# Kernel optimization log

Measured on AMD Instinct MI355X. Metric: run time of the kernel, lower is better.

## Reference

```python
import jax, jax.numpy as jnp
import numpy as np

L, B, C, H = 1024, 8, 1024, 16
D = C // H  # 64


def setup_inputs() -> dict:
    key = jax.random.key(0)
    ks = jax.random.split(key, 8)
    hidden_states = jax.random.normal(ks[0], (L, B, C), dtype=jnp.float32)
    rotary_pos_emb = jax.random.uniform(ks[1], (L, D // 2), dtype=jnp.float32) * 10.0
    attention_mask = jax.random.randint(ks[2], (B, L, L), 0, 2) > 0
    s = 1.0 / np.sqrt(C)
    Wqkv = jax.random.uniform(ks[3], (3 * C, C), dtype=jnp.float32, minval=-s, maxval=s)
    bqkv = jax.random.uniform(ks[4], (3 * C,), dtype=jnp.float32, minval=-s, maxval=s)
    Wo = jax.random.uniform(ks[5], (C, C), dtype=jnp.float32, minval=-s, maxval=s)
    bo = jax.random.uniform(ks[6], (C,), dtype=jnp.float32, minval=-s, maxval=s)
    return {"hidden_states": hidden_states, "rotary_pos_emb": rotary_pos_emb,
            "attention_mask": attention_mask, "Wqkv": Wqkv, "bqkv": bqkv, "Wo": Wo, "bo": bo}


def _rotate_half(x):
    # interleaved pairs: [-x1, x0, -x3, x2, ...]
    x2 = x.reshape(*x.shape[:-1], -1, 2)
    return jnp.stack((-x2[..., 1], x2[..., 0]), axis=-1).reshape(x.shape)


def reference(hidden_states, rotary_pos_emb, attention_mask, Wqkv, bqkv, Wo, bo):
    Lx, Bx, Cx = hidden_states.shape
    # QKV projection: (L,B,3C) -> (3,B,L,H,D)
    qkv = hidden_states @ Wqkv.T + bqkv
    qkv = qkv.reshape(Lx, Bx, 3, H, D).transpose(2, 1, 0, 3, 4)
    q, k, v = qkv[0], qkv[1], qkv[2]  # (B, L, H, D)
    # RoPE: freqs (L, D/2) -> cos/sin (1, L, 1, D) via duplication
    rpe = rotary_pos_emb[None] if rotary_pos_emb.ndim == 2 else rotary_pos_emb
    cos = jnp.concatenate([jnp.cos(rpe), jnp.cos(rpe)], axis=-1)[:, :, None, :]
    sin = jnp.concatenate([jnp.sin(rpe), jnp.sin(rpe)], axis=-1)[:, :, None, :]
    q = q * cos + _rotate_half(q) * sin
    k = k * cos + _rotate_half(k) * sin
    # (B, H, L, D)
    q = q.transpose(0, 2, 1, 3)
    k = k.transpose(0, 2, 1, 3)
    v = v.transpose(0, 2, 1, 3)
    scale = 1.0 / jnp.sqrt(jnp.asarray(D, dtype=q.dtype))
    scores = jnp.einsum('bhqd,bhkd->bhqk', q, k) * scale
    # torch SDPA bool mask: True = attend, False = masked
    scores = jnp.where(attention_mask[:, None, :, :], scores, jnp.finfo(scores.dtype).min)
    attn = jax.nn.softmax(scores, axis=-1)
    out = jnp.einsum('bhqk,bhkd->bhqd', attn, v)  # (B, H, L, D)
    out = out.transpose(2, 0, 1, 3).reshape(Lx, Bx, Cx)  # (L, B, C)
    return out @ Wo.T + bo
```

## Files before the change

### kernel.cpp

```cpp
#include <hip/hip_runtime.h>
#include <hip/hip_bf16.h>

typedef short bf16x8 __attribute__((ext_vector_type(8)));
typedef short bf16x4 __attribute__((ext_vector_type(4)));
typedef float f32x4 __attribute__((ext_vector_type(4)));
typedef unsigned int u32;
typedef unsigned long long u64;

#define GLD_LDS16(gp, lp) \
  __builtin_amdgcn_global_load_lds((const __attribute__((address_space(1))) u32*)(gp), \
                                   (__attribute__((address_space(3))) u32*)(lp), 16, 0, 0)

__device__ __forceinline__ short f2bf(float f) {
  u32 u = __builtin_bit_cast(u32, f);
  u = (u + 0x7fffu + ((u >> 16) & 1u)) >> 16;
  return (short)u;
}

__device__ __forceinline__ u32 pack2_bf16(float a, float b) {
#if __has_builtin(__builtin_amdgcn_cvt_pk_bf16_f32)
  typedef __bf16 bf16v2 __attribute__((ext_vector_type(2)));
  bf16v2 r = __builtin_amdgcn_cvt_pk_bf16_f32(a, b);
  return __builtin_bit_cast(u32, r);
#else
  u32 r;
  asm("v_cvt_pk_bf16_f32 %0, %1, %2" : "=v"(r) : "v"(a), "v"(b));
  return r;
#endif
}

__device__ __forceinline__ float exp2_fast(float x) {
#if __has_builtin(__builtin_amdgcn_exp2f)
  return __builtin_amdgcn_exp2f(x);
#else
  return exp2f(x);
#endif
}

__global__ __launch_bounds__(256) void prep_all(
    const int* __restrict__ m, u64* __restrict__ maskb,
    const float* __restrict__ hs, const float* __restrict__ wqkv,
    const float* __restrict__ wo, short* __restrict__ xb,
    short* __restrict__ wqkvb, short* __restrict__ wob,
    const float* __restrict__ rpe, float* __restrict__ cosT,
    float* __restrict__ sinT) {
  int b = blockIdx.x;
  if (b < 32768) {
    int i = b * 256 + threadIdx.x;
    u64 bm = __ballot(m[i] != 0);
    if ((threadIdx.x & 63) == 0) maskb[i >> 6] = bm;
    return;
  }
  b -= 32768;
  if (b < 12288) {
    const float* in;
    short* out;
    int base;
    if (b < 8192) {
      in = hs; out = xb; base = b * 1024;
    } else if (b < 8192 + 3072) {
      in = wqkv; out = wqkvb; base = (b - 8192) * 1024;
    } else {
      in = wo; out = wob; base = (b - 11264) * 1024;
    }
    int i = base + threadIdx.x * 4;
    float4 v = *(const float4*)(in + i);
    short4 o;
    o.x = f2bf(v.x); o.y = f2bf(v.y); o.z = f2bf(v.z); o.w = f2bf(v.w);
    *(short4*)(out + i) = o;
    return;
  }
  b -= 12288;
  int i = b * 256 + threadIdx.x;
  float v = rpe[i];
  cosT[i] = cosf(v);
  sinT[i] = sinf(v);
}

__global__ __launch_bounds__(512, 2) void gemm_qkv(
    const short* __restrict__ Xb, const short* __restrict__ Wb,
    const float* __restrict__ bqkv, const float* __restrict__ cosT,
    const float* __restrict__ sinT, short* __restrict__ qb,
    short* __restrict__ kbuf, short* __restrict__ vbuf) {
  __shared__ short lds[3][24576];
  const int tid = threadIdx.x;
  const int wid = tid >> 6, lane = tid & 63;
  const int g = lane >> 4, c = lane & 15;
  const int wm = wid >> 2, wn = wid & 3;
  const int bid = blockIdx.y * 12 + blockIdx.x;
  const int swz = (bid & 7) * 96 + (bid >> 3);
  const int m0 = (swz / 12) * 128, n0 = (swz % 12) * 256;

  f32x4 acc[4][4];
#pragma unroll
  for (int i = 0; i < 4; i++)
#pragma unroll
    for (int j = 0; j < 4; j++) acc[i][j] = (f32x4){0.f, 0.f, 0.f, 0.f};

  const int trow = tid >> 3;
  const int gch = ((tid & 7) ^ (trow & 7)) * 8;
  const short* Ag = Xb + (long)(m0 + trow) * 1024 + gch;
  const short* Bg = Wb + (long)(n0 + trow) * 1024 + gch;
  const int lo = tid * 8;

  const int fA = (wm * 64 + c) * 64;
  const int fB = 8192 + (wn * 64 + c) * 64;
  const int ck0 = (g ^ (c & 7)) * 8;

#define QKV_STG(bs, ko) do { \
    GLD_LDS16(Ag + (ko),              &lds[bs][lo]); \
    GLD_LDS16(Ag + (ko) + 64 * 1024,  &lds[bs][4096 + lo]); \
    GLD_LDS16(Bg + (ko),              &lds[bs][8192 + lo]); \
    GLD_LDS16(Bg + (ko) + 64 * 1024,  &lds[bs][12288 + lo]); \
    GLD_LDS16(Bg + (ko) + 128 * 1024, &lds[bs][16384 + lo]); \
    GLD_LDS16(Bg + (ko) + 192 * 1024, &lds[bs][20480 + lo]); \
  } while (0)

  QKV_STG(0, 0);
  QKV_STG(1, 64);
  asm volatile("s_waitcnt vmcnt(6)" ::: "memory");
  __builtin_amdgcn_s_barrier();

  bf16x8 fa[2][4], fb[2][4];
#pragma unroll
  for (int mf = 0; mf < 4; mf++) fa[0][mf] = *(const bf16x8*)&lds[0][fA + mf * 1024 + ck0];
#pragma unroll
  for (int nf = 0; nf < 4; nf++) fb[0][nf] = *(const bf16x8*)&lds[0][fB + nf * 1024 + ck0];

#pragma unroll
  for (int kt = 0; kt < 16; ++kt) {
    const short* Bf = &lds[kt % 3][0];
#pragma unroll
    for (int mf = 0; mf < 4; mf++) fa[1][mf] = *(const bf16x8*)&Bf[fA + mf * 1024 + (ck0 ^ 32)];
#pragma unroll
    for (int nf = 0; nf < 4; nf++) fb[1][nf] = *(const bf16x8*)&Bf[fB + nf * 1024 + (ck0 ^ 32)];
    __builtin_amdgcn_sched_barrier(0);
    __builtin_amdgcn_s_setprio(1);
#pragma unroll
    for (int mf = 0; mf < 4; mf++)
#pragma unroll
      for (int nf = 0; nf < 4; nf++)
        acc[mf][nf] = __builtin_amdgcn_mfma_f32_16x16x32_bf16(fb[0][nf], fa[0][mf], acc[mf][nf], 0, 0, 0);
    __builtin_amdgcn_s_setprio(0);
    __builtin_amdgcn_sched_barrier(0);
    if (kt < 15) {
      asm volatile("s_waitcnt vmcnt(0)" ::: "memory");
      __builtin_amdgcn_s_barrier();
      if (kt < 14) QKV_STG((kt + 2) % 3, (kt + 2) * 64);
      const short* Bn = &lds[(kt + 1) % 3][0];
#pragma unroll
      for (int mf = 0; mf < 4; mf++) fa[0][mf] = *(const bf16x8*)&Bn[fA + mf * 1024 + ck0];
#pragma unroll
      for (int nf = 0; nf < 4; nf++) fb[0][nf] = *(const bf16x8*)&Bn[fB + nf * 1024 + ck0];
      __builtin_amdgcn_sched_barrier(0);
    }
    __builtin_amdgcn_s_setprio(1);
#pragma unroll
    for (int mf = 0; mf < 4; mf++)
#pragma unroll
      for (int nf = 0; nf < 4; nf++)
        acc[mf][nf] = __builtin_amdgcn_mfma_f32_16x16x32_bf16(fb[1][nf], fa[1][mf], acc[mf][nf], 0, 0, 0);
    __builtin_amdgcn_s_setprio(0);
  }
#undef QKV_STG

  for (int jt = 0; jt < 4; jt++) {
    const int chan = n0 + wn * 64 + jt * 16 + g * 4;
    const int three = chan >> 10;
    const int hh = (chan >> 6) & 15;
    const int d = chan & 63;
    const float4 bq = *(const float4*)&bqkv[chan];
    for (int i = 0; i < 4; i++) {
      const int r = m0 + wm * 64 + i * 16 + c;
      const int l = r >> 3, b = r & 7;
      float v0 = acc[i][jt][0] + bq.x;
      float v1 = acc[i][jt][1] + bq.y;
      float v2 = acc[i][jt][2] + bq.z;
      float v3 = acc[i][jt][3] + bq.w;
      const long doff = ((long)(b * 16 + hh) * 1024 + l) * 64 + d;
      if (three == 2) {
        uint2 o = {pack2_bf16(v0, v1), pack2_bf16(v2, v3)};
        *(uint2*)&vbuf[doff] = o;
      } else {
        const float4 cs = *(const float4*)&cosT[l * 32 + (d & 31)];
        const float4 sn = *(const float4*)&sinT[l * 32 + (d & 31)];
        float e0 = v0 * cs.x - v1 * sn.x;
        float o0 = v1 * cs.y + v0 * sn.y;
        float e1 = v2 * cs.z - v3 * sn.z;
        float o1 = v3 * cs.w + v2 * sn.w;
        short* dst;
        if (three == 0) {
          const float S = 0.18033688011f;
          e0 *= S; o0 *= S; e1 *= S; o1 *= S;
          dst = qb;
        } else {
          dst = kbuf;
        }
        uint2 o = {pack2_bf16(e0, o0), pack2_bf16(e1, o1)};
        *(uint2*)&dst[doff] = o;
      }
    }
  }
}

__global__ __launch_bounds__(256) void transpose_v(const short* __restrict__ vbuf,
                                                   short* __restrict__ vTb) {
  __shared__ short T[64 * 72];
  const int bh = blockIdx.y;
  const int l0 = blockIdx.x * 64;
  const int t = threadIdx.x;
  const int row = t >> 3;
  const int cc = (t & 7) * 8;
  const short* src = vbuf + ((long)bh * 1024 + l0) * 64;
  for (int p = 0; p < 2; p++) {
    int lr = row + p * 32;
    *(bf16x8*)&T[lr * 72 + cc] = *(const bf16x8*)&src[(long)lr * 64 + cc];
  }
  __syncthreads();
  short* dst = vTb + (long)bh * 64 * 1024 + l0;
  for (int p = 0; p < 2; p++) {
    int d = row + p * 32;
    bf16x8 v;
    for (int j = 0; j < 8; j++) v[j] = T[(cc + j) * 72 + d];
    *(bf16x8*)&dst[(long)d * 1024 + cc] = v;
  }
}

__global__ __launch_bounds__(256, 5) void flash_attn(
    const short* __restrict__ qb, const short* __restrict__ kbuf,
    const short* __restrict__ vTb, const u64* __restrict__ maskb,
    short* __restrict__ attno) {
  __shared__ short K0[64 * 64], K1[64 * 64];
  __shared__ short V0[64 * 64], V1[64 * 64];
  const int t = threadIdx.x;
  const int wid = t >> 6, lane = t & 63;
  const int g = lane >> 4, c = lane & 15;
  const int bid = blockIdx.y * 16 + blockIdx.x;
  const int swz = (bid & 7) * 256 + (bid >> 3);
  const int q0 = (swz & 15) * 64;
  const int bh = swz >> 4;
  const int b = bh >> 4;
  const int h = bh & 15;
  const long qoff = (long)bh * 1024 * 64;
  const int qrow = q0 + wid * 16 + c;

  bf16x8 aq0, aq1;
  {
    const short* qp = qb + qoff + (long)qrow * 64;
    aq0 = *(const bf16x8*)(qp + g * 8);
    aq1 = *(const bf16x8*)(qp + 32 + g * 8);
  }

  f32x4 Od[4];
  for (int i = 0; i < 4; i++) Od[i] = (f32x4){0.f, 0.f, 0.f, 0.f};
  f32x4 Ld = (f32x4){0.f, 0.f, 0.f, 0.f};
  float m_run = -1e30f;

  bf16x8 avOnes8;
  {
    union { bf16x8 v; u32 u[4]; } av;
    u32 o1 = (c == 0) ? 0x3F803F80u : 0u;
    av.u[0] = av.u[1] = av.u[2] = av.u[3] = o1;
    avOnes8 = av.v;
  }

  const u64* mrow = maskb + ((long)b * 1024 + qrow) * 16;
  const short* Kg = kbuf + qoff;
  const short* Vg = vTb + qoff;

  const int l8 = lane >> 3, l7 = lane & 7;
  const int sr = wid * 16 + l8;
  const int sch = ((l7 ^ l8) & 7) * 8;
  const int r1 = wid * 16 + l8;
  const int r2 = r1 + 8;
  const int kp1 = (r1 & 32) | (((r1 & 15) >> 2) << 3) | (((r1 >> 4) & 1) << 2) | (r1 & 3);
  const int kp2 = (r2 & 32) | (((r2 & 15) >> 2) << 3) | (((r2 >> 4) & 1) << 2) | (r2 & 3);

  const int ck0 = g ^ (c & 7);
  const int kOff0 = c * 64 + ck0 * 8;
  const int kOff1 = c * 64 + (ck0 ^ 4) * 8;
  int vOff32[2];
  for (int kg = 0; kg < 2; kg++)
    vOff32[kg] = c * 64 + (((kg * 4 + g) ^ (c & 7)) * 8);

#define STAGE(KD, VD, ktn) do { \
    GLD_LDS16(Kg + (long)((ktn) + kp1) * 64 + sch,      &KD[(wid * 16) * 64]); \
    GLD_LDS16(Kg + (long)((ktn) + kp2) * 64 + sch,      &KD[(wid * 16 + 8) * 64]); \
    GLD_LDS16(Vg + (long)sr * 1024 + (ktn) + sch,       &VD[(wid * 16) * 64]); \
    GLD_LDS16(Vg + (long)(sr + 8) * 1024 + (ktn) + sch, &VD[(wid * 16 + 8) * 64]); \
  } while (0)

#define TILE(KB, VB, KP, VP, ki) do { \
    u64 mw = mrow[ki]; \
    __syncthreads(); \
    STAGE(KP, VP, (((ki) + 1) & 15) * 64); \
    f32x4 z[4]; \
    for (int nt = 0; nt < 4; nt++) { \
      bf16x8 bk0 = *(const bf16x8*)&KB[kOff0 + nt * 1024]; \
      bf16x8 bk1 = *(const bf16x8*)&KB[kOff1 + nt * 1024]; \
      f32x4 zz = (f32x4){0.f, 0.f, 0.f, 0.f}; \
      zz = __builtin_amdgcn_mfma_f32_16x16x32_bf16(bk0, aq0, zz, 0, 0, 0); \
      zz = __builtin_amdgcn_mfma_f32_16x16x32_bf16(bk1, aq1, zz, 0, 0, 0); \
      z[nt] = zz; \
    } \
    float mx = fmaxf(fmaxf(fmaxf(z[0][0], z[0][1]), fmaxf(z[0][2], z[0][3])), \
                     fmaxf(fmaxf(z[1][0], z[1][1]), fmaxf(z[1][2], z[1][3]))); \
    mx = fmaxf(mx, fmaxf(fmaxf(fmaxf(z[2][0], z[2][1]), fmaxf(z[2][2], z[2][3])), \
                         fmaxf(fmaxf(z[3][0], z[3][1]), fmaxf(z[3][2], z[3][3])))); \
    if (__ballot(mx > m_run + 8.f)) { \
      mx = fmaxf(mx, __shfl_xor(mx, 16, 64)); \
      mx = fmaxf(mx, __shfl_xor(mx, 32, 64)); \
      float mnew = fmaxf(m_run, mx); \
      float al = exp2_fast(m_run - mnew); \
      for (int dt = 0; dt < 4; dt++) { \
        Od[dt][0] *= al; Od[dt][1] *= al; Od[dt][2] *= al; Od[dt][3] *= al; \
      } \
      Ld[0] *= al; \
      m_run = mnew; \
    } \
    for (int kg = 0; kg < 2; kg++) { \
      union { bf16x8 v; u32 u[4]; } pu; \
      for (int ntp = 0; ntp < 2; ntp++) { \
        const int nt = kg * 2 + ntp; \
        u32 m4 = (u32)(mw >> (kg * 32 + g * 8 + ntp * 4)) & 0xFu; \
        u32 mlo = ((m4 & 1u) ? 0xFFFFu : 0u) | ((m4 & 2u) ? 0xFFFF0000u : 0u); \
        u32 mhi = ((m4 & 4u) ? 0xFFFFu : 0u) | ((m4 & 8u) ? 0xFFFF0000u : 0u); \
        float p0 = exp2_fast(z[nt][0] - m_run); \
        float p1 = exp2_fast(z[nt][1] - m_run); \
        float p2 = exp2_fast(z[nt][2] - m_run); \
        float p3 = exp2_fast(z[nt][3] - m_run); \
        pu.u[ntp * 2 + 0] = pack2_bf16(p0, p1) & mlo; \
        pu.u[ntp * 2 + 1] = pack2_bf16(p2, p3) & mhi; \
      } \
      Ld = __builtin_amdgcn_mfma_f32_16x16x32_bf16(avOnes8, pu.v, Ld, 0, 0, 0); \
      for (int dt = 0; dt < 4; dt++) { \
        bf16x8 av = *(const bf16x8*)&VB[vOff32[kg] + dt * 1024]; \
        Od[dt] = __builtin_amdgcn_mfma_f32_16x16x32_bf16(av, pu.v, Od[dt], 0, 0, 0); \
      } \
    } \
  } while (0)

  STAGE(K0, V0, 0);
  for (int ki = 0; ki < 16; ki += 2) {
    TILE(K0, V0, K1, V1, ki);
    TILE(K1, V1, K0, V0, ki + 1);
  }
#undef TILE
#undef STAGE

  float lsum = __shfl(Ld[0], c, 64);
  float inv = 1.f / lsum;
  long rbase = ((long)qrow * 8 + b) * 1024 + h * 64 + g * 4;
  for (int dt = 0; dt < 4; dt++) {
    union { bf16x4 v; u32 u[2]; } o;
    o.u[0] = pack2_bf16(Od[dt][0] * inv, Od[dt][1] * inv);
    o.u[1] = pack2_bf16(Od[dt][2] * inv, Od[dt][3] * inv);
    *(bf16x4*)&attno[rbase + dt * 16] = o.v;
  }
}

__global__ __launch_bounds__(256, 3) void gemm_out(
    const short* __restrict__ Ab, const short* __restrict__ Wob,
    const float* __restrict__ bo, float* __restrict__ out) {
  __shared__ short Ash[3][4096];
  __shared__ short Bsh[3][4096];
  const int tid = threadIdx.x;
  const int wid = tid >> 6, lane = tid & 63;
  const int g = lane >> 4, c = lane & 15;
  const int wm = wid >> 1, wn = wid & 1;
  const int bid = blockIdx.y * 8 + blockIdx.x;
  const int swz = (bid & 7) * 64 + (bid >> 3);
  const int m0 = (swz >> 3) * 128, n0 = (swz & 7) * 128;

  f32x4 acc[4][4];
#pragma unroll
  for (int i = 0; i < 4; i++)
#pragma unroll
    for (int j = 0; j < 4; j++) acc[i][j] = (f32x4){0.f, 0.f, 0.f, 0.f};

  const int srow = lane >> 2;
  const int scol = ((lane & 3) ^ ((lane >> 3) & 3)) * 8;
  const short* AgL = Ab + (long)(m0 + wid * 32 + srow) * 1024 + scol;
  const short* BgL = Wob + (long)(n0 + wid * 32 + srow) * 1024 + scol;
  const int dst0 = (wid * 32) * 32;
  const int dst1 = (wid * 32 + 16) * 32;
  const int ck = g ^ ((c >> 1) & 3);

#define OUT_STG(bs, ko) do { \
    GLD_LDS16(AgL + (ko), &Ash[bs][dst0]); \
    GLD_LDS16(AgL + (ko) + 16 * 1024, &Ash[bs][dst1]); \
    GLD_LDS16(BgL + (ko), &Bsh[bs][dst0]); \
    GLD_LDS16(BgL + (ko) + 16 * 1024, &Bsh[bs][dst1]); \
  } while (0)

  OUT_STG(0, 0);
  OUT_STG(1, 32);
  asm volatile("s_waitcnt vmcnt(4)" ::: "memory");
  __builtin_amdgcn_s_barrier();

  bf16x8 af[2][4], bfr[2][4];
#pragma unroll
  for (int i = 0; i < 4; i++)
    af[0][i] = *(const bf16x8*)&Ash[0][(wm * 64 + i * 16 + c) * 32 + ck * 8];
#pragma unroll
  for (int j = 0; j < 4; j++)
    bfr[0][j] = *(const bf16x8*)&Bsh[0][(wn * 64 + j * 16 + c) * 32 + ck * 8];

#pragma unroll
  for (int kt = 0; kt < 32; ++kt) {
    const int cur = kt & 1, nxt = cur ^ 1;
    __builtin_amdgcn_s_setprio(1);
#pragma unroll
    for (int i = 0; i < 2; i++)
#pragma unroll
      for (int j = 0; j < 4; j++)
        acc[i][j] = __builtin_amdgcn_mfma_f32_16x16x32_bf16(af[cur][i], bfr[cur][j], acc[i][j], 0, 0, 0);
    __builtin_amdgcn_s_setprio(0);
    __builtin_amdgcn_sched_barrier(0);
    if (kt < 31) {
      asm volatile("s_waitcnt vmcnt(0)" ::: "memory");
      __builtin_amdgcn_s_barrier();
      if (kt < 30) OUT_STG((kt + 2) % 3, (kt + 2) * 32);
      const int bn = (kt + 1) % 3;
#pragma unroll
      for (int i = 0; i < 4; i++)
        af[nxt][i] = *(const bf16x8*)&Ash[bn][(wm * 64 + i * 16 + c) * 32 + ck * 8];
#pragma unroll
      for (int j = 0; j < 4; j++)
        bfr[nxt][j] = *(const bf16x8*)&Bsh[bn][(wn * 64 + j * 16 + c) * 32 + ck * 8];
      __builtin_amdgcn_sched_barrier(0);
    }
    __builtin_amdgcn_s_setprio(1);
#pragma unroll
    for (int i = 2; i < 4; i++)
#pragma unroll
      for (int j = 0; j < 4; j++)
        acc[i][j] = __builtin_amdgcn_mfma_f32_16x16x32_bf16(af[cur][i], bfr[cur][j], acc[i][j], 0, 0, 0);
    __builtin_amdgcn_s_setprio(0);
  }
#undef OUT_STG

  for (int jt = 0; jt < 4; jt++) {
    const int j = n0 + wn * 64 + jt * 16 + c;
    const float bias = bo[j];
    for (int i = 0; i < 4; i++) {
      const int rbase = m0 + wm * 64 + i * 16 + g * 4;
      for (int reg = 0; reg < 4; reg++)
        out[(long)(rbase + reg) * 1024 + j] = acc[i][jt][reg] + bias;
    }
  }
}

extern "C" void kernel_launch(void* const* d_in, const int* in_sizes, int n_in,
                              void* d_out, int out_size, void* d_ws, size_t ws_size,
                              hipStream_t stream) {
  const float* hs = (const float*)d_in[0];
  const float* rpe = (const float*)d_in[1];
  const int* amask = (const int*)d_in[2];
  const float* Wqkv = (const float*)d_in[3];
  const float* bqkv = (const float*)d_in[4];
  const float* Wo = (const float*)d_in[5];
  const float* bo = (const float*)d_in[6];
  float* out = (float*)d_out;

  char* ws = (char*)d_ws;
  auto alloc = [&](size_t bytes) {
    char* p = ws;
    ws += (bytes + 255) & ~(size_t)255;
    return p;
  };
  short* Xb = (short*)alloc(8192LL * 1024 * 2);
  short* Wqkvb = (short*)alloc(3072LL * 1024 * 2);
  short* Wob = (short*)alloc(1024LL * 1024 * 2);
  float* cosT = (float*)alloc(1024 * 32 * 4);
  float* sinT = (float*)alloc(1024 * 32 * 4);
  u64* maskb = (u64*)alloc(8LL * 1024 * 16 * 8);
  short* qb = (short*)alloc(128LL * 1024 * 64 * 2);
  short* kbuf = (short*)alloc(128LL * 1024 * 64 * 2);
  short* vbuf = (short*)alloc(128LL * 1024 * 64 * 2);
  short* vTb = (short*)alloc(128LL * 1024 * 64 * 2);
  short* attno = (short*)alloc(8192LL * 1024 * 2);

  prep_all<<<45184, 256, 0, stream>>>(amask, maskb, hs, Wqkv, Wo, Xb, Wqkvb, Wob,
                                      rpe, cosT, sinT);
  gemm_qkv<<<dim3(12, 64), 512, 0, stream>>>(Xb, Wqkvb, bqkv, cosT, sinT, qb, kbuf, vbuf);
  transpose_v<<<dim3(16, 128), 256, 0, stream>>>(vbuf, vTb);
  flash_attn<<<dim3(16, 128), 256, 0, stream>>>(qb, kbuf, vTb, maskb, attno);
  gemm_out<<<dim3(8, 64), 256, 0, stream>>>(attno, Wob, bo, out);
}
```

Baseline: 304.3 us.

## Store attention mask as bytes and expand with v_perm in flash attention

The prep kernel now converts the int mask to one byte per element using vectorized int4 loads, replacing the ballot-packed bitmask. Flash attention reads 8 mask bytes per row segment and expands them into bf16 lane masks with v_perm_b32, instead of the shift/select bit logic. It also adds s_setprio around the MFMA sections and reorders P computation into two full groups. The trade-off is that the mask buffer grows 8x (8 MB versus 1 MB), which adds global reads inside the attention loop in exchange for cheaper ALU work and fewer prep blocks.

```diff
diff --git a/kernel.cpp b/kernel.cpp
--- a/kernel.cpp
+++ b/kernel.cpp
@@ -37,21 +37,32 @@
 #endif
 }
 
+__device__ __forceinline__ u32 bytemask2(u32 src, u32 sel) {
+  u32 r;
+  asm("v_perm_b32 %0, %1, %1, %2" : "=v"(r) : "v"(src), "v"(sel));
+  return r;
+}
+
 __global__ __launch_bounds__(256) void prep_all(
-    const int* __restrict__ m, u64* __restrict__ maskb,
+    const int* __restrict__ m, unsigned char* __restrict__ maskt,
     const float* __restrict__ hs, const float* __restrict__ wqkv,
     const float* __restrict__ wo, short* __restrict__ xb,
     short* __restrict__ wqkvb, short* __restrict__ wob,
     const float* __restrict__ rpe, float* __restrict__ cosT,
     float* __restrict__ sinT) {
   int b = blockIdx.x;
-  if (b < 32768) {
-    int i = b * 256 + threadIdx.x;
-    u64 bm = __ballot(m[i] != 0);
-    if ((threadIdx.x & 63) == 0) maskb[i >> 6] = bm;
+  if (b < 8192) {
+    int i = b * 1024 + threadIdx.x * 4;
+    int4 v = *(const int4*)(m + i);
+    uchar4 o;
+    o.x = v.x ? 0xFFu : 0u;
+    o.y = v.y ? 0xFFu : 0u;
+    o.z = v.z ? 0xFFu : 0u;
+    o.w = v.w ? 0xFFu : 0u;
+    *(uchar4*)(maskt + i) = o;
     return;
   }
-  b -= 32768;
+  b -= 8192;
   if (b < 12288) {
     const float* in;
     short* out;
@@ -228,7 +239,7 @@
 
 __global__ __launch_bounds__(256, 5) void flash_attn(
     const short* __restrict__ qb, const short* __restrict__ kbuf,
-    const short* __restrict__ vTb, const u64* __restrict__ maskb,
+    const short* __restrict__ vTb, const unsigned char* __restrict__ maskt,
     short* __restrict__ attno) {
   __shared__ short K0[64 * 64], K1[64 * 64];
   __shared__ short V0[64 * 64], V1[64 * 64];
@@ -244,6 +255,9 @@
   const long qoff = (long)bh * 1024 * 64;
   const int qrow = q0 + wid * 16 + c;
 
+  const u32 SEL01 = 0x01010000u;
+  const u32 SEL23 = 0x03030202u;
+
   bf16x8 aq0, aq1;
   {
     const short* qp = qb + qoff + (long)qrow * 64;
@@ -264,7 +278,7 @@
     avOnes8 = av.v;
   }
 
-  const u64* mrow = maskb + ((long)b * 1024 + qrow) * 16;
+  const unsigned char* mrow8 = maskt + ((long)b * 1024 + qrow) * 1024 + g * 8;
   const short* Kg = kbuf + qoff;
   const short* Vg = vTb + qoff;
 
@@ -291,10 +305,13 @@
   } while (0)
 
 #define TILE(KB, VB, KP, VP, ki) do { \
-    u64 mw = mrow[ki]; \
-    __syncthreads(); \
+    __syncthreads();  \
     STAGE(KP, VP, (((ki) + 1) & 15) * 64); \
+     \
+    const uint2 w0 = *(const uint2*)&mrow8[(ki) * 64]; \
+    const uint2 w1 = *(const uint2*)&mrow8[(ki) * 64 + 32]; \
     f32x4 z[4]; \
+    __builtin_amdgcn_s_setprio(1); \
     for (int nt = 0; nt < 4; nt++) { \
       bf16x8 bk0 = *(const bf16x8*)&KB[kOff0 + nt * 1024]; \
       bf16x8 bk1 = *(const bf16x8*)&KB[kOff1 + nt * 1024]; \
@@ -303,11 +320,12 @@
       zz = __builtin_amdgcn_mfma_f32_16x16x32_bf16(bk1, aq1, zz, 0, 0, 0); \
       z[nt] = zz; \
     } \
+    __builtin_amdgcn_s_setprio(0); \
     float mx = fmaxf(fmaxf(fmaxf(z[0][0], z[0][1]), fmaxf(z[0][2], z[0][3])), \
                      fmaxf(fmaxf(z[1][0], z[1][1]), fmaxf(z[1][2], z[1][3]))); \
     mx = fmaxf(mx, fmaxf(fmaxf(fmaxf(z[2][0], z[2][1]), fmaxf(z[2][2], z[2][3])), \
                          fmaxf(fmaxf(z[3][0], z[3][1]), fmaxf(z[3][2], z[3][3])))); \
-    if (__ballot(mx > m_run + 8.f)) { \
+    if (__ballot(mx > m_run + 8.f)) {  \
       mx = fmaxf(mx, __shfl_xor(mx, 16, 64)); \
       mx = fmaxf(mx, __shfl_xor(mx, 32, 64)); \
       float mnew = fmaxf(m_run, mx); \
@@ -318,26 +336,39 @@
       Ld[0] *= al; \
       m_run = mnew; \
     } \
-    for (int kg = 0; kg < 2; kg++) { \
-      union { bf16x8 v; u32 u[4]; } pu; \
-      for (int ntp = 0; ntp < 2; ntp++) { \
-        const int nt = kg * 2 + ntp; \
-        u32 m4 = (u32)(mw >> (kg * 32 + g * 8 + ntp * 4)) & 0xFu; \
-        u32 mlo = ((m4 & 1u) ? 0xFFFFu : 0u) | ((m4 & 2u) ? 0xFFFF0000u : 0u); \
-        u32 mhi = ((m4 & 4u) ? 0xFFFFu : 0u) | ((m4 & 8u) ? 0xFFFF0000u : 0u); \
-        float p0 = exp2_fast(z[nt][0] - m_run); \
-        float p1 = exp2_fast(z[nt][1] - m_run); \
-        float p2 = exp2_fast(z[nt][2] - m_run); \
-        float p3 = exp2_fast(z[nt][3] - m_run); \
-        pu.u[ntp * 2 + 0] = pack2_bf16(p0, p1) & mlo; \
-        pu.u[ntp * 2 + 1] = pack2_bf16(p2, p3) & mhi; \
-      } \
-      Ld = __builtin_amdgcn_mfma_f32_16x16x32_bf16(avOnes8, pu.v, Ld, 0, 0, 0); \
-      for (int dt = 0; dt < 4; dt++) { \
-        bf16x8 av = *(const bf16x8*)&VB[vOff32[kg] + dt * 1024]; \
-        Od[dt] = __builtin_amdgcn_mfma_f32_16x16x32_bf16(av, pu.v, Od[dt], 0, 0, 0); \
-      } \
+    union { bf16x8 v; u32 u[4]; } puA, puB; \
+    { \
+      float p0 = exp2_fast(z[0][0] - m_run), p1 = exp2_fast(z[0][1] - m_run); \
+      float p2 = exp2_fast(z[0][2] - m_run), p3 = exp2_fast(z[0][3] - m_run); \
+      float p4 = exp2_fast(z[1][0] - m_run), p5 = exp2_fast(z[1][1] - m_run); \
+      float p6 = exp2_fast(z[1][2] - m_run), p7 = exp2_fast(z[1][3] - m_run); \
+      puA.u[0] = pack2_bf16(p0, p1) & bytemask2(w0.x, SEL01); \
+      puA.u[1] = pack2_bf16(p2, p3) & bytemask2(w0.x, SEL23); \
+      puA.u[2] = pack2_bf16(p4, p5) & bytemask2(w0.y, SEL01); \
+      puA.u[3] = pack2_bf16(p6, p7) & bytemask2(w0.y, SEL23); \
     } \
+    { \
+      float p0 = exp2_fast(z[2][0] - m_run), p1 = exp2_fast(z[2][1] - m_run); \
+      float p2 = exp2_fast(z[2][2] - m_run), p3 = exp2_fast(z[2][3] - m_run); \
+      float p4 = exp2_fast(z[3][0] - m_run), p5 = exp2_fast(z[3][1] - m_run); \
+      float p6 = exp2_fast(z[3][2] - m_run), p7 = exp2_fast(z[3][3] - m_run); \
+      puB.u[0] = pack2_bf16(p0, p1) & bytemask2(w1.x, SEL01); \
+      puB.u[1] = pack2_bf16(p2, p3) & bytemask2(w1.x, SEL23); \
+      puB.u[2] = pack2_bf16(p4, p5) & bytemask2(w1.y, SEL01); \
+      puB.u[3] = pack2_bf16(p6, p7) & bytemask2(w1.y, SEL23); \
+    } \
+    __builtin_amdgcn_s_setprio(1); \
+    Ld = __builtin_amdgcn_mfma_f32_16x16x32_bf16(avOnes8, puA.v, Ld, 0, 0, 0); \
+    for (int dt = 0; dt < 4; dt++) { \
+      bf16x8 av = *(const bf16x8*)&VB[vOff32[0] + dt * 1024]; \
+      Od[dt] = __builtin_amdgcn_mfma_f32_16x16x32_bf16(av, puA.v, Od[dt], 0, 0, 0); \
+    } \
+    Ld = __builtin_amdgcn_mfma_f32_16x16x32_bf16(avOnes8, puB.v, Ld, 0, 0, 0); \
+    for (int dt = 0; dt < 4; dt++) { \
+      bf16x8 av = *(const bf16x8*)&VB[vOff32[1] + dt * 1024]; \
+      Od[dt] = __builtin_amdgcn_mfma_f32_16x16x32_bf16(av, puB.v, Od[dt], 0, 0, 0); \
+    } \
+    __builtin_amdgcn_s_setprio(0); \
   } while (0)
 
   STAGE(K0, V0, 0);
@@ -474,17 +505,17 @@
   short* Wob = (short*)alloc(1024LL * 1024 * 2);
   float* cosT = (float*)alloc(1024 * 32 * 4);
   float* sinT = (float*)alloc(1024 * 32 * 4);
-  u64* maskb = (u64*)alloc(8LL * 1024 * 16 * 8);
+  unsigned char* maskt = (unsigned char*)alloc(8LL * 1024 * 1024);
   short* qb = (short*)alloc(128LL * 1024 * 64 * 2);
   short* kbuf = (short*)alloc(128LL * 1024 * 64 * 2);
   short* vbuf = (short*)alloc(128LL * 1024 * 64 * 2);
   short* vTb = (short*)alloc(128LL * 1024 * 64 * 2);
   short* attno = (short*)alloc(8192LL * 1024 * 2);
 
-  prep_all<<<45184, 256, 0, stream>>>(amask, maskb, hs, Wqkv, Wo, Xb, Wqkvb, Wob,
+  prep_all<<<20608, 256, 0, stream>>>(amask, maskt, hs, Wqkv, Wo, Xb, Wqkvb, Wob,
                                       rpe, cosT, sinT);
   gemm_qkv<<<dim3(12, 64), 512, 0, stream>>>(Xb, Wqkvb, bqkv, cosT, sinT, qb, kbuf, vbuf);
   transpose_v<<<dim3(16, 128), 256, 0, stream>>>(vbuf, vTb);
-  flash_attn<<<dim3(16, 128), 256, 0, stream>>>(qb, kbuf, vTb, maskb, attno);
+  flash_attn<<<dim3(16, 128), 256, 0, stream>>>(qb, kbuf, vTb, maskt, attno);
   gemm_out<<<dim3(8, 64), 256, 0, stream>>>(attno, Wob, bo, out);
 }
```

New measurement: 286.3 us. 5.9% less time.
